# Performance work log

Hardware: AMD Instinct MI355X
Metric: run time of the kernel (lower is better)

Reference implementation:

```python
import jax, jax.numpy as jnp
import numpy as np

NHID = 128
NLAYERS = 4
DT = 1.0
ALPHA = 1.0
GAMMA = 1.0


def setup_inputs() -> dict:
    key = jax.random.key(0)
    k1, k2, k3, k4, k5, k6 = jax.random.split(key, 6)
    N, E = 100000, 1600000
    stdv = 1.0 / np.sqrt(NHID)
    x = jax.random.normal(k1, (N, NHID), dtype=jnp.float32)
    edge_index = jax.random.randint(k2, (2, E), 0, N, dtype=jnp.int64)
    # GCNConv.lin weight (no bias) and separate conv bias; reset_params uniform(-stdv, stdv) for weights
    W = jax.random.uniform(k3, (NHID, NHID), jnp.float32, -stdv, stdv)
    b = jnp.zeros((NHID,), jnp.float32)
    Wres = jax.random.uniform(k4, (NHID, NHID), jnp.float32, -stdv, stdv)
    bres = jax.random.uniform(k5, (NHID,), jnp.float32, -stdv, stdv)
    return {"x": x, "edge_index": edge_index, "W": W, "b": b, "Wres": Wres, "bres": bres}


def reference(x, edge_index, W, b, Wres, bres):
    N = x.shape[0]
    src, dst = edge_index[0], edge_index[1]
    # GCN degree normalization with self-loops (A_hat = A + I)
    deg = jax.ops.segment_sum(jnp.ones(src.shape[0], x.dtype), dst, num_segments=N) + 1.0
    dinv = jax.lax.rsqrt(deg)  # deg >= 1 from self-loops

    def conv(X):
        h = X @ W  # lin (no bias)
        norm = (dinv[src] * dinv[dst])[:, None]
        msg = h[src] * norm                      # [E, nhid] gather
        agg = jax.ops.segment_sum(msg, dst, num_segments=N)  # scatter-add
        agg = agg + h * (dinv * dinv)[:, None]   # self-loop contribution
        return agg + b

    def residual(X):
        # res_connection_v1: -res(conv.lin(X))
        return -((X @ W) @ Wres + bres)

    # dropout is identity in eval mode
    Y = jnp.tanh(x)
    X = Y
    for _ in range(NLAYERS):
        Y = Y + DT * (jnp.tanh(conv(X) + residual(X)) - ALPHA * Y - GAMMA * X)
        X = X + DT * Y
    return X
```

## Files before the change

### kernel.cpp

```cpp
#include <hip/hip_runtime.h>
#include <hip/hip_bf16.h>
#include <stdint.h>

#define THREADS 256
#define WB 256
#define MAXNB 512
#define NBLK_A 512

typedef unsigned short u16;
typedef unsigned int u32;
using frag_ab = __attribute__((ext_vector_type(8))) short;
using f32x4  = __attribute__((ext_vector_type(4))) float;

static __host__ __device__ inline int imin(int a, int b) { return a < b ? a : b; }

static __device__ inline u16 f2b(float f) {
    u32 u = __builtin_bit_cast(u32, f);
    return (u16)((u + 0x7FFFu + ((u >> 16) & 1u)) >> 16);
}
static __device__ inline float b2f_lo(u32 v) { return __builtin_bit_cast(float, v << 16); }
static __device__ inline float b2f_hi(u32 v) { return __builtin_bit_cast(float, v & 0xFFFF0000u); }

static __device__ inline float tanh_fast(float x) {
    const float e = __builtin_amdgcn_exp2f(x * 2.8853900817779268f);
    return 1.0f - 2.0f * __builtin_amdgcn_rcpf(e + 1.0f);
}

static __device__ inline void fma8(float* a, float w, uint4 v) {
    a[0] = fmaf(w, b2f_lo(v.x), a[0]); a[1] = fmaf(w, b2f_hi(v.x), a[1]);
    a[2] = fmaf(w, b2f_lo(v.y), a[2]); a[3] = fmaf(w, b2f_hi(v.y), a[3]);
    a[4] = fmaf(w, b2f_lo(v.z), a[4]); a[5] = fmaf(w, b2f_hi(v.z), a[5]);
    a[6] = fmaf(w, b2f_lo(v.w), a[6]); a[7] = fmaf(w, b2f_hi(v.w), a[7]);
}

static __device__ inline bool detect64(const int* raw) {
    __shared__ int s64;
    if (threadIdx.x == 0) s64 = 1;
    __syncthreads();
    if (raw[2 * threadIdx.x + 1] != 0) s64 = 0;
    __syncthreads();
    return s64 != 0;
}

__global__ __launch_bounds__(256)
void k_bucket_count(const int* __restrict__ raw, int E, int EPB, int NB,
                    int* __restrict__ counts) {
    const bool is64 = detect64(raw);
    __shared__ int cnt[MAXNB];
    const int t = threadIdx.x, blk = blockIdx.x;
    for (int i = t; i < NB; i += THREADS) cnt[i] = 0;
    __syncthreads();
    const int e0 = blk * EPB, e1 = imin(E, e0 + EPB);
    for (int e = e0 + t; e < e1; e += THREADS) {
        const int d = is64 ? raw[2 * E + 2 * e] : raw[E + e];
        atomicAdd(&cnt[d >> 8], 1);
    }
    __syncthreads();
    for (int i = t; i < NB; i += THREADS) counts[i * NBLK_A + blk] = cnt[i];
}

__global__ void k_chunk_sums(const int* __restrict__ a, int* __restrict__ chunkSum, int L) {
    __shared__ int sm[THREADS];
    const int base = blockIdx.x * 2048 + threadIdx.x * 8;
    int s = 0;
#pragma unroll
    for (int i = 0; i < 8; ++i) { int idx = base + i; if (idx < L) s += a[idx]; }
    sm[threadIdx.x] = s;
    __syncthreads();
    for (int off = THREADS / 2; off > 0; off >>= 1) {
        if (threadIdx.x < off) sm[threadIdx.x] += sm[threadIdx.x + off];
        __syncthreads();
    }
    if (threadIdx.x == 0) chunkSum[blockIdx.x] = sm[0];
}

__global__ void k_scan_offsets(const int* __restrict__ chunkSum, int* __restrict__ chunkOff,
                               int nChunks) {
    if (blockIdx.x == 0 && threadIdx.x == 0) {
        int run = 0;
        for (int i = 0; i < nChunks; ++i) { chunkOff[i] = run; run += chunkSum[i]; }
    }
}

__global__ void k_scan_write(int* __restrict__ a, const int* __restrict__ chunkOff, int L) {
    __shared__ int sm[THREADS];
    const int tid = threadIdx.x;
    const int base = blockIdx.x * 2048 + tid * 8;
    int v[8]; int s = 0;
#pragma unroll
    for (int i = 0; i < 8; ++i) { int idx = base + i; v[i] = (idx < L) ? a[idx] : 0; s += v[i]; }
    const int mysum = s;
    sm[tid] = s;
    __syncthreads();
    for (int off = 1; off < THREADS; off <<= 1) {
        int t = (tid >= off) ? sm[tid - off] : 0;
        __syncthreads();
        sm[tid] += t;
        __syncthreads();
    }
    int run = chunkOff[blockIdx.x] + sm[tid] - mysum;
#pragma unroll
    for (int i = 0; i < 8; ++i) {
        int idx = base + i;
        if (idx < L) { a[idx] = run; run += v[i]; }
    }
}

__global__ __launch_bounds__(256)
void k_bucket_scatter(const int* __restrict__ raw, int E, int EPB, int NB,
                      const int* __restrict__ offs, uint2* __restrict__ pairs) {
    const bool is64 = detect64(raw);
    __shared__ int cur[MAXNB];
    const int t = threadIdx.x, blk = blockIdx.x;
    for (int i = t; i < NB; i += THREADS) cur[i] = offs[i * NBLK_A + blk];
    __syncthreads();
    const int e0 = blk * EPB, e1 = imin(E, e0 + EPB);
    for (int e = e0 + t; e < e1; e += THREADS) {
        int s, d;
        if (is64) { s = raw[2 * e]; d = raw[2 * E + 2 * e]; }
        else      { s = raw[e];     d = raw[E + e]; }
        const int p = atomicAdd(&cur[d >> 8], 1);
        pairs[p] = make_uint2((u32)s, (u32)d);
    }
}

__global__ __launch_bounds__(256)
void k_build(const uint2* __restrict__ pairs, const int* __restrict__ offs,
             int* __restrict__ rowptr, int* __restrict__ csr_src,
             float* __restrict__ dinv, int N, int NB, int E) {
    __shared__ int deg[WB];
    __shared__ int ptr[WB];
    __shared__ int cur[WB];
    const int k = blockIdx.x, t = threadIdx.x;
    const int base = offs[k * NBLK_A];
    const int end  = (k + 1 < NB) ? offs[(k + 1) * NBLK_A] : E;
    const int n0 = k * WB;
    deg[t] = 0;
    __syncthreads();
    for (int e = base + t; e < end; e += THREADS)
        atomicAdd(&deg[(int)pairs[e].y - n0], 1);
    __syncthreads();
    const int dv = deg[t];
    if (n0 + t < N) dinv[n0 + t] = rsqrtf((float)dv + 1.0f);
    ptr[t] = dv;
    __syncthreads();
    for (int off = 1; off < THREADS; off <<= 1) {
        int v = (t >= off) ? ptr[t - off] : 0;
        __syncthreads();
        ptr[t] += v;
        __syncthreads();
    }
    const int excl = ptr[t] - dv;
    if (n0 + t < N) rowptr[n0 + t] = base + excl;
    if (k == NB - 1 && t == 0) rowptr[N] = E;
    cur[t] = excl;
    __syncthreads();
    for (int e = base + t; e < end; e += THREADS) {
        const uint2 pr = pairs[e];
        const int p = atomicAdd(&cur[(int)pr.y - n0], 1);
        csr_src[base + p] = (int)pr.x;
    }
}

__global__ void k_wfill(const int* __restrict__ csr_src, const float* __restrict__ dinv,
                        uint2* __restrict__ csrW, int E) {
    int i = blockIdx.x * blockDim.x + threadIdx.x;
    const int st = gridDim.x * blockDim.x;
    for (; i < E; i += st) {
        const int s = csr_src[i];
        csrW[i] = make_uint2((u32)s, __builtin_bit_cast(u32, dinv[s]));
    }
}

__global__ void k_w2(const float* __restrict__ W, const float* __restrict__ Wres,
                     const float* __restrict__ b, const float* __restrict__ bres,
                     u16* __restrict__ Bt, float* __restrict__ cvec) {
    const int gid = blockIdx.x * blockDim.x + threadIdx.x;
    if (gid < 128 * 128) {
        const int i = gid >> 7, n = gid & 127;
        float s = 0.f;
#pragma unroll 8
        for (int k = 0; k < 128; ++k) s += W[i * 128 + k] * Wres[k * 128 + n];
        Bt[n * 256 + 128 + i] = f2b(-s);
        Bt[n * 256 + i]       = f2b(W[i * 128 + n]);
    }
    if (gid < 128) cvec[gid] = b[gid] - bres[gid];
}

__global__ void k_tanh0(const float* __restrict__ x, u16* __restrict__ Xh, long long n4) {
    long long i = blockIdx.x * (long long)blockDim.x + threadIdx.x;
    const long long stride = gridDim.x * (long long)blockDim.x;
    for (; i < n4; i += stride) {
        float4 v = ((const float4*)x)[i];
        u32 lo = f2b(tanh_fast(v.x)) | ((u32)f2b(tanh_fast(v.y)) << 16);
        u32 hi = f2b(tanh_fast(v.z)) | ((u32)f2b(tanh_fast(v.w)) << 16);
        ((uint2*)Xh)[i] = make_uint2(lo, hi);
    }
}

__global__ __launch_bounds__(256)
void k_agg(const u16* __restrict__ Xh, const int* __restrict__ rowptr,
           const uint2* __restrict__ csrW, u16* __restrict__ Ph, int N) {
    const int qid = threadIdx.x >> 4;
    const int l16 = threadIdx.x & 15;
    const int node = blockIdx.x * 16 + qid;
    const bool valid = node < N;
    const int c8 = l16 * 8;
    int e0 = 0, e1 = 0;
    if (valid) { e0 = rowptr[node]; e1 = rowptr[node + 1]; }
    const float dn = rsqrtf((float)(e1 - e0) + 1.0f);
    float acc[8] = {0.f, 0.f, 0.f, 0.f, 0.f, 0.f, 0.f, 0.f};
    if (valid) {
        const uint4 v = *(const uint4*)&Xh[(size_t)node * 128 + c8];
        fma8(acc, dn, v);
    }
    int e = e0;
    for (; e + 3 < e1; e += 4) {
        const uint2 cw0 = csrW[e],     cw1 = csrW[e + 1];
        const uint2 cw2 = csrW[e + 2], cw3 = csrW[e + 3];
        const uint4 v0 = *(const uint4*)&Xh[(size_t)cw0.x * 128 + c8];
        const uint4 v1 = *(const uint4*)&Xh[(size_t)cw1.x * 128 + c8];
        const uint4 v2 = *(const uint4*)&Xh[(size_t)cw2.x * 128 + c8];
        const uint4 v3 = *(const uint4*)&Xh[(size_t)cw3.x * 128 + c8];
        fma8(acc, __builtin_bit_cast(float, cw0.y), v0);
        fma8(acc, __builtin_bit_cast(float, cw1.y), v1);
        fma8(acc, __builtin_bit_cast(float, cw2.y), v2);
        fma8(acc, __builtin_bit_cast(float, cw3.y), v3);
    }
    for (; e < e1; ++e) {
        const uint2 cw = csrW[e];
        const uint4 v = *(const uint4*)&Xh[(size_t)cw.x * 128 + c8];
        fma8(acc, __builtin_bit_cast(float, cw.y), v);
    }
    if (valid) {
        u32 w0 = (u32)f2b(acc[0] * dn) | ((u32)f2b(acc[1] * dn) << 16);
        u32 w1 = (u32)f2b(acc[2] * dn) | ((u32)f2b(acc[3] * dn) << 16);
        u32 w2 = (u32)f2b(acc[4] * dn) | ((u32)f2b(acc[5] * dn) << 16);
        u32 w3 = (u32)f2b(acc[6] * dn) | ((u32)f2b(acc[7] * dn) << 16);
        *(uint4*)&Ph[(size_t)node * 128 + c8] = make_uint4(w0, w1, w2, w3);
    }
}

__global__ __launch_bounds__(256)
void k_gemm_mfma(const u16* __restrict__ Ph, const u16* __restrict__ Xh,
                 const u16* __restrict__ Bt, const float* __restrict__ cvec,
                 float* __restrict__ Xout, u16* __restrict__ XhOut, int M, int writeF32) {
    __shared__ u16 Bs[128 * 128];
    const int tid = threadIdx.x;
    const int wid = tid >> 6, lane = tid & 63;
    const int rowbase = blockIdx.x * 128 + wid * 32;
    const int rl = lane & 15;
    const int kg = (lane >> 4) * 8;

    const int r0 = rowbase + rl;
    const size_t ar0 = (size_t)((r0      < M) ? r0      : M - 1);
    const size_t ar1 = (size_t)((r0 + 16 < M) ? r0 + 16 : M - 1);

    frag_ab a0[8], a1[8];
#pragma unroll
    for (int ks = 0; ks < 4; ++ks) {
        const int kk = ks * 32 + kg;
        a0[ks]     = *(const frag_ab*)&Ph[ar0 * 128 + kk];
        a1[ks]     = *(const frag_ab*)&Ph[ar1 * 128 + kk];
        a0[ks + 4] = *(const frag_ab*)&Xh[ar0 * 128 + kk];
        a1[ks + 4] = *(const frag_ab*)&Xh[ar1 * 128 + kk];
    }

    f32x4 acc[2][8];
#pragma unroll
    for (int i = 0; i < 2; ++i)
#pragma unroll
        for (int j = 0; j < 8; ++j) acc[i][j] = (f32x4){0.f, 0.f, 0.f, 0.f};

#pragma unroll
    for (int half = 0; half < 2; ++half) {
#pragma unroll
        for (int p = 0; p < 8; ++p) {
            const int c = p * 256 + tid;
            const int row = c >> 4, c16 = c & 15;
            const uint4 v = *(const uint4*)&Bt[row * 256 + half * 128 + c16 * 8];
            *(uint4*)&Bs[row * 128 + (((c16 * 16) ^ ((row & 7) << 4)) >> 1)] = v;
        }
        __syncthreads();
#pragma unroll
        for (int ks = 0; ks < 4; ++ks) {
            const int kb = ks * 64 + kg * 2;
#pragma unroll
            for (int nf = 0; nf < 8; ++nf) {
                const int r = nf * 16 + rl;
                const frag_ab bv = *(const frag_ab*)&Bs[r * 128 + ((kb ^ ((r & 7) << 4)) >> 1)];
                acc[0][nf] = __builtin_amdgcn_mfma_f32_16x16x32_bf16(a0[half * 4 + ks], bv,
                                                                      acc[0][nf], 0, 0, 0);
                acc[1][nf] = __builtin_amdgcn_mfma_f32_16x16x32_bf16(a1[half * 4 + ks], bv,
                                                                      acc[1][nf], 0, 0, 0);
            }
        }
        __syncthreads();
    }

    const int rq = (lane >> 4) * 4;
    if (writeF32) {
#pragma unroll
        for (int mf = 0; mf < 2; ++mf)
#pragma unroll
            for (int nf = 0; nf < 8; ++nf) {
                const int c = nf * 16 + rl;
                const float cv = cvec[c];
#pragma unroll
                for (int reg = 0; reg < 4; ++reg) {
                    const int r = rowbase + mf * 16 + rq + reg;
                    if (r < M) Xout[(size_t)r * 128 + c] = tanh_fast(acc[mf][nf][reg] + cv);
                }
            }
    } else {
#pragma unroll
        for (int mf = 0; mf < 2; ++mf)
#pragma unroll
            for (int nf = 0; nf < 8; ++nf) {
                const int c = nf * 16 + rl;
                const float cv = cvec[c];
#pragma unroll
                for (int reg = 0; reg < 4; ++reg) {
                    const int rloc = wid * 32 + mf * 16 + rq + reg;
                    Bs[rloc * 128 + (c ^ ((rloc & 7) << 3))] =
                        f2b(tanh_fast(acc[mf][nf][reg] + cv));
                }
            }
        __syncthreads();
#pragma unroll
        for (int k = 0; k < 8; ++k) {
            const int ci = k * 256 + tid;
            const int row = ci >> 4, c8 = ci & 15;
            const int gr = blockIdx.x * 128 + row;
            if (gr < M) {
                const uint4 v = *(const uint4*)&Bs[row * 128 + ((c8 * 8) ^ ((row & 7) << 3))];
                *(uint4*)&XhOut[(size_t)gr * 128 + c8 * 8] = v;
            }
        }
    }
}

extern "C" void kernel_launch(void* const* d_in, const int* in_sizes, int n_in,
                              void* d_out, int out_size, void* d_ws, size_t ws_size,
                              hipStream_t stream) {
    const float* x    = (const float*)d_in[0];
    const int*   ei   = (const int*)d_in[1];
    const float* W    = (const float*)d_in[2];
    const float* b    = (const float*)d_in[3];
    const float* Wres = (const float*)d_in[4];
    const float* bres = (const float*)d_in[5];
    const int N = in_sizes[0] / 128;
    const int E = in_sizes[1] / 2;
    float* X = (float*)d_out;

    uint8_t* base = (uint8_t*)d_ws;
    size_t off = 0;
    auto carve = [&](size_t bytes) -> void* {
        void* p = base + off;
        off += (bytes + 255) & ~(size_t)255;
        return p;
    };
    const int NB = imin((N + WB - 1) / WB, MAXNB);
    const int L = NB * NBLK_A;

    u16*   Xh       = (u16*)carve((size_t)N * 128 * sizeof(u16));
    u16*   Ph       = (u16*)carve((size_t)N * 128 * sizeof(u16));
    uint2* pairs    = (uint2*)carve((size_t)E * sizeof(uint2));
    uint2* csrW     = pairs;
    int*   csr_src  = (int*)carve((size_t)E * sizeof(int));
    int*   counts   = (int*)carve((size_t)L * sizeof(int));
    int*   rowptr   = (int*)carve(((size_t)N + 1) * sizeof(int));
    float* dinv     = (float*)carve((size_t)N * sizeof(float));
    u16*   Bt       = (u16*)carve(128 * 256 * sizeof(u16));
    float* cvec     = (float*)carve(128 * sizeof(float));
    int*   chunkSum = (int*)carve(4096);
    int*   chunkOff = (int*)carve(4096);

    const int EPB = (E + NBLK_A - 1) / NBLK_A;
    const int nChunks = (L + 2047) / 2048;

    k_bucket_count<<<NBLK_A, THREADS, 0, stream>>>(ei, E, EPB, NB, counts);
    k_chunk_sums<<<nChunks, THREADS, 0, stream>>>(counts, chunkSum, L);
    k_scan_offsets<<<1, 64, 0, stream>>>(chunkSum, chunkOff, nChunks);
    k_scan_write<<<nChunks, THREADS, 0, stream>>>(counts, chunkOff, L);
    k_bucket_scatter<<<NBLK_A, THREADS, 0, stream>>>(ei, E, EPB, NB, counts, pairs);
    k_build<<<NB, THREADS, 0, stream>>>(pairs, counts, rowptr, csr_src, dinv, N, NB, E);
    k_wfill<<<2048, THREADS, 0, stream>>>(csr_src, dinv, csrW, E);
    k_w2<<<64, THREADS, 0, stream>>>(W, Wres, b, bres, Bt, cvec);

    const long long n4 = (long long)N * 32;
    const int tgrid = imin((int)((n4 + THREADS - 1) / THREADS), 2048);
    k_tanh0<<<tgrid, THREADS, 0, stream>>>(x, Xh, n4);

    for (int l = 0; l < 4; ++l) {
        k_agg<<<(N + 15) / 16, THREADS, 0, stream>>>(Xh, rowptr, csrW, Ph, N);
        k_gemm_mfma<<<(N + 127) / 128, THREADS, 0, stream>>>(Ph, Xh, Bt, cvec, X, Xh, N,
                                                             (l == 3) ? 1 : 0);
    }
}
```

Before: 425.0 us.

## Degree-sort nodes within buckets and deepen edge prefetch in aggregation

Measured after the change: 482.1 us. +13.4%, slower.

```diff
diff --git a/kernel.cpp b/kernel.cpp
--- a/kernel.cpp
+++ b/kernel.cpp
@@ -108,7 +108,7 @@
 
 __global__ __launch_bounds__(256)
 void k_bucket_scatter(const int* __restrict__ raw, int E, int EPB, int NB,
-                      const int* __restrict__ offs, uint2* __restrict__ pairs) {
+                      const int* __restrict__ offs, u32* __restrict__ pairs) {
     const bool is64 = detect64(raw);
     __shared__ int cur[MAXNB];
     const int t = threadIdx.x, blk = blockIdx.x;
@@ -120,16 +120,18 @@
         if (is64) { s = raw[2 * e]; d = raw[2 * E + 2 * e]; }
         else      { s = raw[e];     d = raw[E + e]; }
         const int p = atomicAdd(&cur[d >> 8], 1);
-        pairs[p] = make_uint2((u32)s, (u32)d);
+        pairs[p] = (u32)s | ((u32)(d & 255) << 24);
     }
 }
 
 __global__ __launch_bounds__(256)
-void k_build(const uint2* __restrict__ pairs, const int* __restrict__ offs,
-             int* __restrict__ rowptr, int* __restrict__ csr_src,
+void k_build(const u32* __restrict__ pairs, const int* __restrict__ offs,
+             int* __restrict__ rowptrP, int* __restrict__ perm, int* __restrict__ csr_src,
              float* __restrict__ dinv, int N, int NB, int E) {
     __shared__ int deg[WB];
-    __shared__ int ptr[WB];
+    __shared__ int rnk[WB];
+    __shared__ int degR[WB];
+    __shared__ int scanR[WB];
     __shared__ int cur[WB];
     const int k = blockIdx.x, t = threadIdx.x;
     const int base = offs[k * NBLK_A];
@@ -138,27 +140,35 @@
     deg[t] = 0;
     __syncthreads();
     for (int e = base + t; e < end; e += THREADS)
-        atomicAdd(&deg[(int)pairs[e].y - n0], 1);
+        atomicAdd(&deg[pairs[e] >> 24], 1);
     __syncthreads();
     const int dv = deg[t];
     if (n0 + t < N) dinv[n0 + t] = rsqrtf((float)dv + 1.0f);
-    ptr[t] = dv;
-    __syncthreads();
-    for (int off = 1; off < THREADS; off <<= 1) {
-        int v = (t >= off) ? ptr[t - off] : 0;
-        __syncthreads();
-        ptr[t] += v;
-        __syncthreads();
-    }
-    const int excl = ptr[t] - dv;
-    if (n0 + t < N) rowptr[n0 + t] = base + excl;
-    if (k == NB - 1 && t == 0) rowptr[N] = E;
-    cur[t] = excl;
+    int r = 0;
+    for (int u = 0; u < WB; ++u) {
+        const int du = deg[u];
+        r += (du < dv) || (du == dv && u < t);
+    }
+    rnk[t] = r;
+    degR[r] = dv;
+    __syncthreads();
+    scanR[t] = degR[t];
+    __syncthreads();
+    for (int off = 1; off < WB; off <<= 1) {
+        int v = (t >= off) ? scanR[t - off] : 0;
+        __syncthreads();
+        scanR[t] += v;
+        __syncthreads();
+    }
+    rowptrP[k * WB + t] = base + scanR[t] - degR[t];
+    if (k == NB - 1 && t == 0) rowptrP[NB * WB] = E;
+    perm[k * WB + r] = (n0 + t < N) ? (n0 + t) : -1;
+    cur[t] = base + scanR[r] - dv;
     __syncthreads();
     for (int e = base + t; e < end; e += THREADS) {
-        const uint2 pr = pairs[e];
-        const int p = atomicAdd(&cur[(int)pr.y - n0], 1);
-        csr_src[base + p] = (int)pr.x;
+        const u32 w = pairs[e];
+        const int p = atomicAdd(&cur[w >> 24], 1);
+        csr_src[p] = (int)(w & 0xFFFFFF);
     }
 }
 
@@ -199,40 +209,52 @@
 }
 
 __global__ __launch_bounds__(256)
-void k_agg(const u16* __restrict__ Xh, const int* __restrict__ rowptr,
-           const uint2* __restrict__ csrW, u16* __restrict__ Ph, int N) {
+void k_agg(const u16* __restrict__ Xh, const int* __restrict__ rowptrP,
+           const int* __restrict__ perm, const uint2* __restrict__ csrW,
+           u16* __restrict__ Ph) {
     const int qid = threadIdx.x >> 4;
     const int l16 = threadIdx.x & 15;
-    const int node = blockIdx.x * 16 + qid;
-    const bool valid = node < N;
+    const int g = blockIdx.x * 16 + qid;
+    const int node = perm[g];
+    const int e0 = rowptrP[g], e1 = rowptrP[g + 1];
     const int c8 = l16 * 8;
-    int e0 = 0, e1 = 0;
-    if (valid) { e0 = rowptr[node]; e1 = rowptr[node + 1]; }
     const float dn = rsqrtf((float)(e1 - e0) + 1.0f);
     float acc[8] = {0.f, 0.f, 0.f, 0.f, 0.f, 0.f, 0.f, 0.f};
-    if (valid) {
+    if (node >= 0) {
         const uint4 v = *(const uint4*)&Xh[(size_t)node * 128 + c8];
         fma8(acc, dn, v);
     }
     int e = e0;
-    for (; e + 3 < e1; e += 4) {
-        const uint2 cw0 = csrW[e],     cw1 = csrW[e + 1];
-        const uint2 cw2 = csrW[e + 2], cw3 = csrW[e + 3];
-        const uint4 v0 = *(const uint4*)&Xh[(size_t)cw0.x * 128 + c8];
-        const uint4 v1 = *(const uint4*)&Xh[(size_t)cw1.x * 128 + c8];
-        const uint4 v2 = *(const uint4*)&Xh[(size_t)cw2.x * 128 + c8];
-        const uint4 v3 = *(const uint4*)&Xh[(size_t)cw3.x * 128 + c8];
-        fma8(acc, __builtin_bit_cast(float, cw0.y), v0);
-        fma8(acc, __builtin_bit_cast(float, cw1.y), v1);
-        fma8(acc, __builtin_bit_cast(float, cw2.y), v2);
-        fma8(acc, __builtin_bit_cast(float, cw3.y), v3);
+    if (e + 8 <= e1) {
+        uint2 cw[8];
+#pragma unroll
+        for (int i = 0; i < 8; ++i) cw[i] = csrW[e + i];
+        while (true) {
+            uint4 v[8];
+#pragma unroll
+            for (int i = 0; i < 8; ++i)
+                v[i] = *(const uint4*)&Xh[(size_t)cw[i].x * 128 + c8];
+            e += 8;
+            const bool more = (e + 8 <= e1);
+            uint2 nw[8];
+            if (more) {
+#pragma unroll
+                for (int i = 0; i < 8; ++i) nw[i] = csrW[e + i];
+            }
+#pragma unroll
+            for (int i = 0; i < 8; ++i)
+                fma8(acc, __builtin_bit_cast(float, cw[i].y), v[i]);
+            if (!more) break;
+#pragma unroll
+            for (int i = 0; i < 8; ++i) cw[i] = nw[i];
+        }
     }
     for (; e < e1; ++e) {
         const uint2 cw = csrW[e];
         const uint4 v = *(const uint4*)&Xh[(size_t)cw.x * 128 + c8];
         fma8(acc, __builtin_bit_cast(float, cw.y), v);
     }
-    if (valid) {
+    if (node >= 0) {
         u32 w0 = (u32)f2b(acc[0] * dn) | ((u32)f2b(acc[1] * dn) << 16);
         u32 w1 = (u32)f2b(acc[2] * dn) | ((u32)f2b(acc[3] * dn) << 16);
         u32 w2 = (u32)f2b(acc[4] * dn) | ((u32)f2b(acc[5] * dn) << 16);
@@ -362,14 +384,16 @@
     };
     const int NB = imin((N + WB - 1) / WB, MAXNB);
     const int L = NB * NBLK_A;
+    const int NPOS = NB * WB;
 
     u16*   Xh       = (u16*)carve((size_t)N * 128 * sizeof(u16));
     u16*   Ph       = (u16*)carve((size_t)N * 128 * sizeof(u16));
-    uint2* pairs    = (uint2*)carve((size_t)E * sizeof(uint2));
-    uint2* csrW     = pairs;
+    u32*   pairs    = (u32*)carve((size_t)E * sizeof(u32));
+    uint2* csrW     = (uint2*)carve((size_t)E * sizeof(uint2));
     int*   csr_src  = (int*)carve((size_t)E * sizeof(int));
     int*   counts   = (int*)carve((size_t)L * sizeof(int));
-    int*   rowptr   = (int*)carve(((size_t)N + 1) * sizeof(int));
+    int*   rowptrP  = (int*)carve(((size_t)NPOS + 1) * sizeof(int));
+    int*   perm     = (int*)carve((size_t)NPOS * sizeof(int));
     float* dinv     = (float*)carve((size_t)N * sizeof(float));
     u16*   Bt       = (u16*)carve(128 * 256 * sizeof(u16));
     float* cvec     = (float*)carve(128 * sizeof(float));
@@ -384,7 +408,7 @@
     k_scan_offsets<<<1, 64, 0, stream>>>(chunkSum, chunkOff, nChunks);
     k_scan_write<<<nChunks, THREADS, 0, stream>>>(counts, chunkOff, L);
     k_bucket_scatter<<<NBLK_A, THREADS, 0, stream>>>(ei, E, EPB, NB, counts, pairs);
-    k_build<<<NB, THREADS, 0, stream>>>(pairs, counts, rowptr, csr_src, dinv, N, NB, E);
+    k_build<<<NB, THREADS, 0, stream>>>(pairs, counts, rowptrP, perm, csr_src, dinv, N, NB, E);
     k_wfill<<<2048, THREADS, 0, stream>>>(csr_src, dinv, csrW, E);
     k_w2<<<64, THREADS, 0, stream>>>(W, Wres, b, bres, Bt, cvec);
 
@@ -393,7 +417,7 @@
     k_tanh0<<<tgrid, THREADS, 0, stream>>>(x, Xh, n4);
 
     for (int l = 0; l < 4; ++l) {
-        k_agg<<<(N + 15) / 16, THREADS, 0, stream>>>(Xh, rowptr, csrW, Ph, N);
+        k_agg<<<NB * 16, THREADS, 0, stream>>>(Xh, rowptrP, perm, csrW, Ph);
         k_gemm_mfma<<<(N + 127) / 128, THREADS, 0, stream>>>(Ph, Xh, Bt, cvec, X, Xh, N,
                                                              (l == 3) ? 1 : 0);
     }
```
